# Kernel tuning notes

Hardware: AMD Instinct MI355X
Metric: run time of the kernel (lower is better)

The kernel has to match this reference:

```python
import jax, jax.numpy as jnp
import numpy as np

NUM_HEADS = 16
NEG = -1e9


def setup_inputs() -> dict:
    key = jax.random.key(0)
    k_x, k_w1, k_w2, k_b, k_p = jax.random.split(key, 5)
    B, T, C = 4, 2048, 1024
    x = jax.random.normal(k_x, (B, T, C), dtype=jnp.float32)
    # nn.Linear default init ~ U(-1/sqrt(fan_in), 1/sqrt(fan_in)); stored as (in, out) for x @ W
    s = 1.0 / np.sqrt(C)
    Wqkv = jax.random.uniform(k_w1, (C, 3 * C), minval=-s, maxval=s, dtype=jnp.float32)
    Wout = jax.random.uniform(k_w2, (C, C), minval=-s, maxval=s, dtype=jnp.float32)
    bout = jax.random.uniform(k_b, (C,), minval=-s, maxval=s, dtype=jnp.float32)
    perm = jax.random.permutation(k_p, T).astype(jnp.int32)
    return {"x": x, "Wqkv": Wqkv, "Wout": Wout, "bout": bout, "perm": perm}


def reference(x, Wqkv, Wout, bout, perm):
    B, T, C = x.shape
    H = NUM_HEADS
    D = C // H
    qkv = x @ Wqkv                                   # [B,T,3C]
    q, k, v = jnp.split(qkv, 3, axis=-1)
    q = q.reshape(B, T, H, D)
    k = k.reshape(B, T, H, D)
    v = v.reshape(B, T, H, D)
    scale = 1.0 / jnp.sqrt(jnp.asarray(D, dtype=x.dtype))
    scores = jnp.einsum('bqhd,bkhd->bhqk', q, k) * scale   # [B,H,T,T]
    # permuted causal mask: allowed[i, j] = tril[i, perm[j]] = (perm[j] <= i)
    i = jnp.arange(T)[:, None]
    bias = jnp.where(perm[None, :] <= i, 0.0, NEG).astype(x.dtype)  # [T,T]
    attn = jax.nn.softmax(scores + bias[None, None, :, :], axis=-1)
    out = jnp.einsum('bhqk,bkhd->bqhd', attn, v).reshape(B, T, C)
    return out @ Wout + bout
```

## Files before the change

kernel.cpp:

```cpp
#include <hip/hip_runtime.h>
#include <stdint.h>
#include <stddef.h>

#define BSZ   4
#define TSEQ  2048
#define CDIM  1024
#define HEADS 16
#define DHEAD 64

typedef __attribute__((ext_vector_type(8))) short v8s;
typedef __attribute__((ext_vector_type(4))) float v4f;

__device__ __forceinline__ v4f mfma16(v8s a, v8s b, v4f c) {
  return __builtin_amdgcn_mfma_f32_16x16x32_bf16(a, b, c, 0, 0, 0);
}

__device__ __forceinline__ short f2bf(float f) {
  union { float f; uint32_t u; } v; v.f = f;
  uint32_t r = (v.u + 0x7FFFu + ((v.u >> 16) & 1u)) >> 16;
  return (short)(uint16_t)r;
}

__device__ __forceinline__ uint32_t cvt_pk_bf16(float lo, float hi) {
  uint32_t r;
  asm("v_cvt_pk_bf16_f32 %0, %1, %2" : "=v"(r) : "v"(lo), "v"(hi));
  return r;
}

__device__ __forceinline__ void gl_lds16(const void* g, void* l) {
  __builtin_amdgcn_global_load_lds((const __attribute__((address_space(1))) void*)g,
                                   (__attribute__((address_space(3))) void*)l, 16, 0, 0);
}

#define BARw __builtin_amdgcn_s_barrier()
#define LGKM0 do { asm volatile("s_waitcnt lgkmcnt(0)" ::: "memory"); \
                   __builtin_amdgcn_sched_barrier(0); } while (0)

__global__ __launch_bounds__(256) void k_convert(const float* __restrict__ in,
                                                 short* __restrict__ out, int n) {
  int i = (blockIdx.x * 256 + threadIdx.x) * 4;
  if (i >= n) return;
  float4 v = *(const float4*)(in + i);
  short4 o;
  o.x = f2bf(v.x); o.y = f2bf(v.y); o.z = f2bf(v.z); o.w = f2bf(v.w);
  *(short4*)(out + i) = o;
}

__global__ __launch_bounds__(256) void k_transpose_conv(const float* __restrict__ in,
                                                        short* __restrict__ out,
                                                        int R, int C) {
  __shared__ float tile[32][33];
  int c0 = blockIdx.x * 32, r0 = blockIdx.y * 32;
  int tx = threadIdx.x, ty = threadIdx.y;
  #pragma unroll
  for (int i = ty; i < 32; i += 8)
    tile[i][tx] = in[(size_t)(r0 + i) * C + c0 + tx];
  __syncthreads();
  #pragma unroll
  for (int i = ty; i < 32; i += 8)
    out[(size_t)(c0 + i) * R + r0 + tx] = f2bf(tile[tx][i]);
}

__global__ __launch_bounds__(256) void k_vt(const short* __restrict__ Vs,
                                            short* __restrict__ Vt) {
  __shared__ short tl[64][72];
  const int t0 = blockIdx.x * 64, h = blockIdx.y, b = blockIdx.z;
  const int row = threadIdx.x >> 2, c4 = threadIdx.x & 3;
  const short* src = Vs + (size_t)(b * TSEQ + t0 + row) * CDIM + h * DHEAD;
  #pragma unroll
  for (int it = 0; it < 2; ++it) {
    int ch = c4 + it * 4;
    *(v8s*)&tl[row][ch * 8] = *(const v8s*)(src + ch * 8);
  }
  __syncthreads();
  short* dst = Vt + ((size_t)(b * HEADS + h) * DHEAD + row) * TSEQ + t0;
  #pragma unroll
  for (int it = 0; it < 2; ++it) {
    int ch = c4 + it * 4;
    v8s o;
    #pragma unroll
    for (int j = 0; j < 8; ++j) o[j] = tl[ch * 8 + j][row];
    *(v8s*)(dst + ch * 8) = o;
  }
}

__global__ __launch_bounds__(512, 2) void k_gemm_qkv(const short* __restrict__ A,
                                                     const short* __restrict__ Wt,
                                                     const int* __restrict__ perm,
                                                     short* __restrict__ QK,
                                                     short* __restrict__ Vs) {
  __shared__ __align__(16) short Alds[2][256 * 64];
  __shared__ __align__(16) short Blds[2][256 * 64];
  const int l = threadIdx.x & 63, w = threadIdx.x >> 6;
  const int lr = l & 15, lg = l >> 4;
  const int wm = w >> 2, wn = w & 3;
  const int bid = blockIdx.x;
  const int swz = (bid & 7) * 48 + (bid >> 3);
  const int by = swz / 12, bx = swz - by * 12;
  const int row0 = by * 256, col0 = bx * 256;

  v4f acc[8][4];
  #pragma unroll
  for (int i = 0; i < 8; ++i)
    #pragma unroll
    for (int j = 0; j < 4; ++j) acc[i][j] = (v4f){0.f, 0.f, 0.f, 0.f};

  const int rowoff = w * 8 + (l >> 3);
  const int gch = ((l & 7) ^ (l >> 3)) * 16;
  const char* Asrc = (const char*)A  + (size_t)(row0 + rowoff) * 2048 + gch;
  const char* Bsrc = (const char*)Wt + (size_t)(col0 + rowoff) * 2048 + gch;
  char* AL = (char*)&Alds[0][0];
  char* BL = (char*)&Blds[0][0];
  const int sdst = w * 1024;

  auto SA = [&](int kt, int h, int d) {
    char* dst = AL + d * 32768 + h * 16384 + sdst;
    const char* s = Asrc + (size_t)(h * 128) * 2048 + kt * 128;
    gl_lds16(s, dst);
    gl_lds16(s + (size_t)64 * 2048, dst + 8192);
  };
  auto SB = [&](int kt, int h, int d) {
    char* dst = BL + d * 32768 + h * 16384 + sdst;
    const char* s = Bsrc + (size_t)(h * 128) * 2048 + kt * 128;
    gl_lds16(s, dst);
    gl_lds16(s + (size_t)64 * 2048, dst + 8192);
  };

  const int rsw = (lr & 7) * 16;
  const int koff0 = (lg * 16) ^ rsw;
  const int koff1 = ((4 + lg) * 16) ^ rsw;
  const int abase = (wm * 128 + lr) * 128;
  const int bbase = (wn * 64 + lr) * 128;

  v8s af[4][2], bf[4][2];
  auto RDA = [&](int d, int ih) {
    const char* base = AL + d * 32768 + abase + ih * 8192;
    #pragma unroll
    for (int ii = 0; ii < 4; ++ii) {
      af[ii][0] = *(const v8s*)(base + ii * 2048 + koff0);
      af[ii][1] = *(const v8s*)(base + ii * 2048 + koff1);
    }
  };
  auto RDB = [&](int d) {
    const char* base = BL + d * 32768 + bbase;
    #pragma unroll
    for (int j = 0; j < 4; ++j) {
      bf[j][0] = *(const v8s*)(base + j * 2048 + koff0);
      bf[j][1] = *(const v8s*)(base + j * 2048 + koff1);
    }
  };

#define MMC(IH, JH)                                                            \
  do {                                                                         \
    __builtin_amdgcn_s_setprio(1);                                             \
    _Pragma("unroll")                                                          \
    for (int kk = 0; kk < 2; ++kk)                                             \
      _Pragma("unroll")                                                        \
      for (int ii = 0; ii < 4; ++ii)                                           \
        _Pragma("unroll")                                                      \
        for (int jj = 0; jj < 2; ++jj)                                         \
          acc[(IH) * 4 + ii][(JH) * 2 + jj] =                                  \
              mfma16(af[ii][kk], bf[(JH) * 2 + jj][kk],                        \
                     acc[(IH) * 4 + ii][(JH) * 2 + jj]);                       \
    __builtin_amdgcn_s_setprio(0);                                             \
  } while (0)

  SB(0, 0, 0); SB(0, 1, 0); SA(0, 0, 0); SA(0, 1, 0);
  SB(1, 0, 1); SB(1, 1, 1); SA(1, 0, 1); SA(1, 1, 1);
  asm volatile("s_waitcnt vmcnt(8)" ::: "memory");
  BARw;

  for (int i = 0; i < 8; ++i) {
    const int kt2 = 2 * i + 2, kt3 = 2 * i + 3;
    const bool st = (i < 7);
    RDA(0, 0); RDB(0);
    BARw; LGKM0; MMC(0, 0); BARw;
    if (st) SB(kt2, 0, 0);
    BARw; MMC(0, 1); BARw;
    RDA(0, 1); if (st) SB(kt2, 1, 0);
    BARw; LGKM0; MMC(1, 0); BARw;
    if (st) { SA(kt2, 0, 0); asm volatile("s_waitcnt vmcnt(6)" ::: "memory"); }
    else    { asm volatile("s_waitcnt vmcnt(0)" ::: "memory"); }
    BARw; MMC(1, 1); BARw;
    RDA(1, 0); RDB(1); if (st) SA(kt2, 1, 0);
    BARw; LGKM0; MMC(0, 0); BARw;
    if (st) SB(kt3, 0, 1);
    BARw; MMC(0, 1); BARw;
    RDA(1, 1); if (st) SB(kt3, 1, 1);
    BARw; LGKM0; MMC(1, 0); BARw;
    if (st) {
      SA(kt3, 0, 1); SA(kt3, 1, 1);
      asm volatile("s_waitcnt vmcnt(8)" ::: "memory");
    }
    BARw; MMC(1, 1); BARw;
  }
#undef MMC

  const int region = (col0 + wn * 64) >> 10;
  if (region == 0) {
    #pragma unroll
    for (int i = 0; i < 8; ++i) {
      int rowb = row0 + wm * 128 + i * 16 + lg * 4;
      #pragma unroll
      for (int j = 0; j < 4; ++j) {
        int col = col0 + wn * 64 + j * 16 + lr;
        #pragma unroll
        for (int r = 0; r < 4; ++r)
          QK[(size_t)(rowb + r) * 2048 + col] = f2bf(acc[i][j][r]);
      }
    }
  } else if (region == 1) {
    #pragma unroll
    for (int i = 0; i < 8; ++i) {
      int rowb = row0 + wm * 128 + i * 16 + lg * 4;
      int prow[4];
      #pragma unroll
      for (int r = 0; r < 4; ++r) {
        int t = (rowb + r) & 2047;
        prow[r] = ((rowb + r) - t) + perm[t];
      }
      #pragma unroll
      for (int j = 0; j < 4; ++j) {
        int col = col0 + wn * 64 + j * 16 + lr;
        #pragma unroll
        for (int r = 0; r < 4; ++r)
          QK[(size_t)prow[r] * 2048 + col] = f2bf(acc[i][j][r]);
      }
    }
  } else {
    #pragma unroll
    for (int i = 0; i < 8; ++i) {
      int rowb = row0 + wm * 128 + i * 16 + lg * 4;
      int prow[4];
      #pragma unroll
      for (int r = 0; r < 4; ++r) {
        int t = (rowb + r) & 2047;
        prow[r] = ((rowb + r) - t) + perm[t];
      }
      #pragma unroll
      for (int j = 0; j < 4; ++j) {
        int vc = col0 + wn * 64 + j * 16 + lr - 2048;
        #pragma unroll
        for (int r = 0; r < 4; ++r)
          Vs[(size_t)prow[r] * CDIM + vc] = f2bf(acc[i][j][r]);
      }
    }
  }
}

__global__ __launch_bounds__(256) void k_gemm_out(const short* __restrict__ A,
                                                  const short* __restrict__ Wt,
                                                  const float* __restrict__ bias,
                                                  float* __restrict__ out) {
  __shared__ __align__(16) short As[3][128 * 32];
  __shared__ __align__(16) short Bs[3][128 * 32];
  int l = threadIdx.x & 63, w = threadIdx.x >> 6;
  int lr = l & 15, lg = l >> 4;
  int row0 = blockIdx.y * 128, col0 = blockIdx.x * 128;
  int wr = (w >> 1) * 64, wc = (w & 1) * 64;
  v4f acc[4][4];
  #pragma unroll
  for (int i = 0; i < 4; ++i)
    #pragma unroll
    for (int j = 0; j < 4; ++j) acc[i][j] = (v4f){0.f, 0.f, 0.f, 0.f};

  const short* Ag = A  + (size_t)(row0 + w * 32 + (l >> 2)) * CDIM + (l & 3) * 8;
  const short* Bg = Wt + (size_t)(col0 + w * 32 + (l >> 2)) * CDIM + (l & 3) * 8;
  const int so = (w * 32) * 32;

  auto STAGE = [&](int it, int bf) {
    int k0 = it * 32;
    gl_lds16(Ag + k0, &As[bf][so]);
    gl_lds16(Ag + k0 + 16 * CDIM, &As[bf][so + 16 * 32]);
    gl_lds16(Bg + k0, &Bs[bf][so]);
    gl_lds16(Bg + k0 + 16 * CDIM, &Bs[bf][so + 16 * 32]);
  };

  auto BODY = [&](int it, int cur) {
    if (it < 31) asm volatile("s_waitcnt vmcnt(4)" ::: "memory");
    else         asm volatile("s_waitcnt vmcnt(0)" ::: "memory");
    __builtin_amdgcn_s_barrier();
    if (it < 30) STAGE(it + 2, (cur + 2) % 3);
    v8s af[4], bfr[4];
    #pragma unroll
    for (int i = 0; i < 4; ++i) af[i] = *(const v8s*)&As[cur][(wr + i * 16 + lr) * 32 + lg * 8];
    #pragma unroll
    for (int j = 0; j < 4; ++j) bfr[j] = *(const v8s*)&Bs[cur][(wc + j * 16 + lr) * 32 + lg * 8];
    __builtin_amdgcn_s_setprio(1);
    #pragma unroll
    for (int i = 0; i < 4; ++i)
      #pragma unroll
      for (int j = 0; j < 4; ++j) acc[i][j] = mfma16(af[i], bfr[j], acc[i][j]);
    __builtin_amdgcn_s_setprio(0);
  };

  STAGE(0, 0);
  STAGE(1, 1);
  for (int it = 0; it < 30; it += 3) {
    BODY(it, 0); BODY(it + 1, 1); BODY(it + 2, 2);
  }
  BODY(30, 0);
  BODY(31, 1);

  #pragma unroll
  for (int i = 0; i < 4; ++i) {
    int rowb = row0 + wr + i * 16 + lg * 4;
    #pragma unroll
    for (int j = 0; j < 4; ++j) {
      int col = col0 + wc + j * 16 + lr;
      float bv = bias[col];
      #pragma unroll
      for (int r = 0; r < 4; ++r)
        out[(size_t)(rowb + r) * CDIM + col] = acc[i][j][r] + bv;
    }
  }
}

__global__ __launch_bounds__(512) void k_flash(const short* __restrict__ QK,
                                               const short* __restrict__ Vt,
                                               short* __restrict__ O) {
  __shared__ __align__(16) short Kbuf[3][64 * 64];
  __shared__ __align__(16) short Vbuf[3][64 * 64];
  __shared__ __align__(16) short plds[8][32 * 64];
  const int l = threadIdx.x & 63, w = threadIdx.x >> 6;
  const int lr = l & 15, lg = l >> 4;
  const int n = blockIdx.x;
  const int u = n & 255;
  const int h = u & 15;
  const int b = (u >> 4) & 3;
  const int qi = u >> 6;
  const int qb = (n < 256) ? (7 - qi) : qi;
  const int q0 = qb * 256 + w * 32;
  const int nt = 4 * qb + 4;
  const float C1 = 0.18033688011112042f;

  const short* Qb = QK + (size_t)(b * TSEQ + q0) * 2048 + h * DHEAD;
  v8s aq[2][2];
  #pragma unroll
  for (int hh = 0; hh < 2; ++hh) {
    aq[hh][0] = *(const v8s*)(Qb + (size_t)(hh * 16 + lr) * 2048 + lg * 8);
    aq[hh][1] = *(const v8s*)(Qb + (size_t)(hh * 16 + lr) * 2048 + 32 + lg * 8);
  }

  v8s ones;
  #pragma unroll
  for (int i = 0; i < 8; ++i) ones[i] = (short)0x3F80;

  v4f Oacc[2][4], sacc[2];
  #pragma unroll
  for (int hh = 0; hh < 2; ++hh) {
    sacc[hh] = (v4f){0.f, 0.f, 0.f, 0.f};
    #pragma unroll
    for (int d = 0; d < 4; ++d) Oacc[hh][d] = (v4f){0.f, 0.f, 0.f, 0.f};
  }

  const char* Ksrc = (const char*)QK + (size_t)(b * TSEQ) * 4096 + 2048 + (size_t)h * 128;
  const char* Vsrc = (const char*)Vt + (size_t)((b * HEADS + h) * DHEAD) * 4096;
  const int srow = w * 8 + (l >> 3);
  const int csw  = ((l & 7) ^ (l >> 3)) * 16;

  auto STAGE = [&](int kt, int bf) {
    char* kd = (char*)&Kbuf[bf][0] + w * 1024;
    char* vd = (char*)&Vbuf[bf][0] + w * 1024;
    gl_lds16(Ksrc + ((size_t)kt * 64 + srow) * 4096 + csw, kd);
    gl_lds16(Vsrc + (size_t)srow * 4096 + (size_t)kt * 128 + csw, vd);
  };

  STAGE(0, 0);
  if (nt > 1) STAGE(1, 1);
  const int x16 = (lr & 7) * 16;
  char* pb = (char*)&plds[w][0];
  const int e7 = lr & 7;

  for (int kt = 0; kt < nt; ++kt) {
    const int cur = kt % 3;
    if (kt + 1 < nt) asm volatile("s_waitcnt vmcnt(2)" ::: "memory");
    else             asm volatile("s_waitcnt vmcnt(0)" ::: "memory");
    __builtin_amdgcn_s_barrier();
    if (kt + 2 < nt) STAGE(kt + 2, (kt + 2) % 3);

    if (kt * 64 <= q0 + 31) {
      const char* Kc = (const char*)&Kbuf[cur][0];
      const char* Vc = (const char*)&Vbuf[cur][0];

      v4f S[2][4];
      __builtin_amdgcn_s_setprio(1);
      #pragma unroll
      for (int g = 0; g < 4; ++g) {
        const char* rp = Kc + (g * 16 + lr) * 128;
        v8s k0 = *(const v8s*)(rp + ((lg * 16) ^ x16));
        v8s k1 = *(const v8s*)(rp + ((64 + lg * 16) ^ x16));
        #pragma unroll
        for (int hh = 0; hh < 2; ++hh) {
          v4f z = (v4f){0.f, 0.f, 0.f, 0.f};
          z = mfma16(k0, aq[hh][0], z);
          S[hh][g] = mfma16(k1, aq[hh][1], z);
        }
      }
      __builtin_amdgcn_s_setprio(0);

      if (kt * 64 + 63 <= q0) {
        #pragma unroll
        for (int hh = 0; hh < 2; ++hh) {
          char* rowp = pb + (hh * 16 + lr) * 128 + 8 * (lg & 1);
          #pragma unroll
          for (int g = 0; g < 4; ++g) {
            float p0 = __builtin_exp2f(fmaf(S[hh][g][0], C1, -8.0f));
            float p1 = __builtin_exp2f(fmaf(S[hh][g][1], C1, -8.0f));
            float p2 = __builtin_exp2f(fmaf(S[hh][g][2], C1, -8.0f));
            float p3 = __builtin_exp2f(fmaf(S[hh][g][3], C1, -8.0f));
            uint2 wv;
            wv.x = cvt_pk_bf16(p0, p1);
            wv.y = cvt_pk_bf16(p2, p3);
            *(uint2*)(rowp + (((2 * g + (lg >> 1)) ^ e7) << 4)) = wv;
          }
        }
      } else {
        const int kg0 = kt * 64 + lg * 4;
        #pragma unroll
        for (int hh = 0; hh < 2; ++hh) {
          const int irow = q0 + hh * 16 + lr;
          char* rowp = pb + (hh * 16 + lr) * 128 + 8 * (lg & 1);
          #pragma unroll
          for (int g = 0; g < 4; ++g) {
            float p[4];
            #pragma unroll
            for (int r = 0; r < 4; ++r) {
              float e = __builtin_exp2f(fmaf(S[hh][g][r], C1, -8.0f));
              p[r] = (kg0 + g * 16 + r <= irow) ? e : 0.0f;
            }
            uint2 wv;
            wv.x = cvt_pk_bf16(p[0], p[1]);
            wv.y = cvt_pk_bf16(p[2], p[3]);
            *(uint2*)(rowp + (((2 * g + (lg >> 1)) ^ e7) << 4)) = wv;
          }
        }
      }
      asm volatile("s_waitcnt lgkmcnt(0)" ::: "memory");
      __builtin_amdgcn_sched_barrier(0);

      v8s ap[2][2];
      #pragma unroll
      for (int hh = 0; hh < 2; ++hh) {
        const char* rowp = pb + (hh * 16 + lr) * 128;
        ap[hh][0] = *(const v8s*)(rowp + ((lg ^ e7) << 4));
        ap[hh][1] = *(const v8s*)(rowp + (((4 + lg) ^ e7) << 4));
      }
      __builtin_amdgcn_s_setprio(1);
      #pragma unroll
      for (int hh = 0; hh < 2; ++hh) {
        sacc[hh] = mfma16(ap[hh][0], ones, sacc[hh]);
        sacc[hh] = mfma16(ap[hh][1], ones, sacc[hh]);
      }
      #pragma unroll
      for (int dk = 0; dk < 4; ++dk) {
        const char* vp = Vc + (dk * 16 + lr) * 128;
        v8s bv0 = *(const v8s*)(vp + ((lg * 16) ^ x16));
        v8s bv1 = *(const v8s*)(vp + ((64 + lg * 16) ^ x16));
        #pragma unroll
        for (int hh = 0; hh < 2; ++hh) {
          Oacc[hh][dk] = mfma16(ap[hh][0], bv0, Oacc[hh][dk]);
          Oacc[hh][dk] = mfma16(ap[hh][1], bv1, Oacc[hh][dk]);
        }
      }
      __builtin_amdgcn_s_setprio(0);
    }
  }

  #pragma unroll
  for (int hh = 0; hh < 2; ++hh) {
    float inv[4];
    #pragma unroll
    for (int r = 0; r < 4; ++r) inv[r] = 1.0f / sacc[hh][r];
    #pragma unroll
    for (int dk = 0; dk < 4; ++dk)
      #pragma unroll
      for (int r = 0; r < 4; ++r) {
        int row = q0 + hh * 16 + lg * 4 + r;
        int col = h * DHEAD + dk * 16 + lr;
        O[(size_t)(b * TSEQ + row) * CDIM + col] = f2bf(Oacc[hh][dk][r] * inv[r]);
      }
  }
}

extern "C" void kernel_launch(void* const* d_in, const int* in_sizes, int n_in,
                              void* d_out, int out_size, void* d_ws, size_t ws_size,
                              hipStream_t stream) {
  const float* x    = (const float*)d_in[0];
  const float* Wqkv = (const float*)d_in[1];
  const float* Wout = (const float*)d_in[2];
  const float* bout = (const float*)d_in[3];
  const int*   perm = (const int*)d_in[4];
  float* out = (float*)d_out;

  uint8_t* ws = (uint8_t*)d_ws;
  const size_t NTOK = (size_t)BSZ * TSEQ;
  size_t off = 0;
  short* Xb    = (short*)(ws + off); off += NTOK * CDIM * 2;
  short* Wqkvt = (short*)(ws + off); off += (size_t)3 * CDIM * CDIM * 2;
  short* Woutt = (short*)(ws + off); off += (size_t)CDIM * CDIM * 2;
  short* QKb   = (short*)(ws + off); off += NTOK * 2048 * 2;
  short* Vtb   = (short*)(ws + off); off += NTOK * CDIM * 2;
  short* Obuf  = (short*)(ws + off); off += NTOK * CDIM * 2;
  short* Vsb   = Obuf;

  {
    int n = (int)(NTOK * CDIM);
    k_convert<<<n / (256 * 4), 256, 0, stream>>>(x, Xb, n);
  }
  k_transpose_conv<<<dim3(3 * CDIM / 32, CDIM / 32), dim3(32, 8), 0, stream>>>(Wqkv, Wqkvt, CDIM, 3 * CDIM);
  k_transpose_conv<<<dim3(CDIM / 32, CDIM / 32), dim3(32, 8), 0, stream>>>(Wout, Woutt, CDIM, CDIM);
  k_gemm_qkv<<<dim3((NTOK / 256) * (3 * CDIM / 256)), 512, 0, stream>>>(Xb, Wqkvt, perm, QKb, Vsb);
  k_vt<<<dim3(TSEQ / 64, HEADS, BSZ), 256, 0, stream>>>(Vsb, Vtb);
  k_flash<<<dim3(512), 512, 0, stream>>>(QKb, Vtb, Obuf);
  k_gemm_out<<<dim3(CDIM / 128, NTOK / 128), 256, 0, stream>>>(Obuf, Woutt, bout, out);
}
```

Before: 201.4 us.

## Split long causal query blocks across two KV halves and add combine kernel

The attention kernel splits the key range of the four heaviest query blocks (upper half of the sequence) into two halves, each processed by a separate workgroup. Partial unnormalized outputs and row sums go to scratch buffers, and a new combine kernel adds them and normalizes. The aim is to balance load across a larger grid (768 blocks instead of 512) and shorten the critical path. The cost is an extra launch, the scratch traffic, and rounding the partials to bf16 before they are summed. The scheme relies on fixed softmax without a running max, so partial sums can be added directly.

```diff
diff --git a/kernel.cpp b/kernel.cpp
--- a/kernel.cpp
+++ b/kernel.cpp
@@ -19,6 +19,11 @@
   union { float f; uint32_t u; } v; v.f = f;
   uint32_t r = (v.u + 0x7FFFu + ((v.u >> 16) & 1u)) >> 16;
   return (short)(uint16_t)r;
+}
+
+__device__ __forceinline__ float bf2f(short s) {
+  union { float f; uint32_t u; } v; v.u = ((uint32_t)(uint16_t)s) << 16;
+  return v.f;
 }
 
 __device__ __forceinline__ uint32_t cvt_pk_bf16(float lo, float hi) {
@@ -318,20 +323,27 @@
 
 __global__ __launch_bounds__(512) void k_flash(const short* __restrict__ QK,
                                                const short* __restrict__ Vt,
-                                               short* __restrict__ O) {
+                                               short* __restrict__ O,
+                                               short* __restrict__ Opart,
+                                               float* __restrict__ Spart) {
   __shared__ __align__(16) short Kbuf[3][64 * 64];
   __shared__ __align__(16) short Vbuf[3][64 * 64];
   __shared__ __align__(16) short plds[8][32 * 64];
   const int l = threadIdx.x & 63, w = threadIdx.x >> 6;
   const int lr = l & 15, lg = l >> 4;
   const int n = blockIdx.x;
-  const int u = n & 255;
+  const int grp = n >> 6;
+  const int u = n & 63;
   const int h = u & 15;
-  const int b = (u >> 4) & 3;
-  const int qi = u >> 6;
-  const int qb = (n < 256) ? (7 - qi) : qi;
+  const int b = u >> 4;
+  const bool spl = (grp < 8);
+  const int qb   = spl ? (7 - (grp >> 1)) : (11 - grp);
+  const int half = spl ? (grp & 1) : 0;
+  const int ntf  = 4 * qb + 4;
+  const int kt0  = (spl && half) ? (ntf >> 1) : 0;
+  const int kt1  = (spl && !half) ? (ntf >> 1) : ntf;
+  const int ntl  = kt1 - kt0;
   const int q0 = qb * 256 + w * 32;
-  const int nt = 4 * qb + 4;
   const float C1 = 0.18033688011112042f;
 
   const short* Qb = QK + (size_t)(b * TSEQ + q0) * 2048 + h * DHEAD;
@@ -366,18 +378,19 @@
     gl_lds16(Vsrc + (size_t)srow * 4096 + (size_t)kt * 128 + csw, vd);
   };
 
-  STAGE(0, 0);
-  if (nt > 1) STAGE(1, 1);
+  STAGE(kt0, 0);
+  if (ntl > 1) STAGE(kt0 + 1, 1);
   const int x16 = (lr & 7) * 16;
   char* pb = (char*)&plds[w][0];
   const int e7 = lr & 7;
 
-  for (int kt = 0; kt < nt; ++kt) {
-    const int cur = kt % 3;
-    if (kt + 1 < nt) asm volatile("s_waitcnt vmcnt(2)" ::: "memory");
+  for (int j = 0; j < ntl; ++j) {
+    const int kt = kt0 + j;
+    const int cur = j % 3;
+    if (j + 1 < ntl) asm volatile("s_waitcnt vmcnt(2)" ::: "memory");
     else             asm volatile("s_waitcnt vmcnt(0)" ::: "memory");
     __builtin_amdgcn_s_barrier();
-    if (kt + 2 < nt) STAGE(kt + 2, (kt + 2) % 3);
+    if (j + 2 < ntl) STAGE(kt0 + j + 2, (j + 2) % 3);
 
     if (kt * 64 <= q0 + 31) {
       const char* Kc = (const char*)&Kbuf[cur][0];
@@ -467,20 +480,62 @@
     }
   }
 
-  #pragma unroll
-  for (int hh = 0; hh < 2; ++hh) {
-    float inv[4];
-    #pragma unroll
-    for (int r = 0; r < 4; ++r) inv[r] = 1.0f / sacc[hh][r];
-    #pragma unroll
-    for (int dk = 0; dk < 4; ++dk)
-      #pragma unroll
-      for (int r = 0; r < 4; ++r) {
-        int row = q0 + hh * 16 + lg * 4 + r;
-        int col = h * DHEAD + dk * 16 + lr;
-        O[(size_t)(b * TSEQ + row) * CDIM + col] = f2bf(Oacc[hh][dk][r] * inv[r]);
-      }
-  }
+  if (!spl) {
+    #pragma unroll
+    for (int hh = 0; hh < 2; ++hh) {
+      float inv[4];
+      #pragma unroll
+      for (int r = 0; r < 4; ++r) inv[r] = 1.0f / sacc[hh][r];
+      #pragma unroll
+      for (int dk = 0; dk < 4; ++dk)
+        #pragma unroll
+        for (int r = 0; r < 4; ++r) {
+          int row = q0 + hh * 16 + lg * 4 + r;
+          int col = h * DHEAD + dk * 16 + lr;
+          O[(size_t)(b * TSEQ + row) * CDIM + col] = f2bf(Oacc[hh][dk][r] * inv[r]);
+        }
+    }
+  } else {
+    #pragma unroll
+    for (int hh = 0; hh < 2; ++hh)
+      #pragma unroll
+      for (int dk = 0; dk < 4; ++dk)
+        #pragma unroll
+        for (int r = 0; r < 4; ++r) {
+          int prow = q0 + hh * 16 + lg * 4 + r - 1024;
+          int col = h * DHEAD + dk * 16 + lr;
+          Opart[((size_t)(half * 4 + b) * 1024 + prow) * 1024 + col] = f2bf(Oacc[hh][dk][r]);
+        }
+    if (lr == 0) {
+      #pragma unroll
+      for (int hh = 0; hh < 2; ++hh)
+        #pragma unroll
+        for (int r = 0; r < 4; ++r) {
+          int prow = q0 + hh * 16 + lg * 4 + r - 1024;
+          Spart[((size_t)(half * 4 + b) * 16 + h) * 1024 + prow] = sacc[hh][r];
+        }
+    }
+  }
+}
+
+__global__ __launch_bounds__(256) void k_combine(const short* __restrict__ Opart,
+                                                 const float* __restrict__ Spart,
+                                                 short* __restrict__ O) {
+  int idx = (blockIdx.x * 256 + threadIdx.x) * 8;
+  int row = idx >> 10;
+  int col = idx & 1023;
+  int b = row >> 10, pr = row & 1023;
+  int h = col >> 6;
+  float s = Spart[((size_t)b * 16 + h) * 1024 + pr] +
+            Spart[((size_t)(4 + b) * 16 + h) * 1024 + pr];
+  float inv = 1.0f / s;
+  v8s o0 = *(const v8s*)(Opart + ((size_t)row) * 1024 + col);
+  v8s o1 = *(const v8s*)(Opart + ((size_t)(4096 + row)) * 1024 + col);
+  v8s o;
+  #pragma unroll
+  for (int j = 0; j < 8; ++j)
+    o[j] = f2bf((bf2f(o0[j]) + bf2f(o1[j])) * inv);
+  *(v8s*)(O + ((size_t)(b * TSEQ + 1024 + pr)) * 1024 + col) = o;
 }
 
 extern "C" void kernel_launch(void* const* d_in, const int* in_sizes, int n_in,
@@ -502,7 +557,9 @@
   short* QKb   = (short*)(ws + off); off += NTOK * 2048 * 2;
   short* Vtb   = (short*)(ws + off); off += NTOK * CDIM * 2;
   short* Obuf  = (short*)(ws + off); off += NTOK * CDIM * 2;
+  float* Spart = (float*)(ws + off); off += 2 * 4 * 16 * 1024 * 4;
   short* Vsb   = Obuf;
+  short* Opart = Xb;
 
   {
     int n = (int)(NTOK * CDIM);
@@ -512,6 +569,7 @@
   k_transpose_conv<<<dim3(CDIM / 32, CDIM / 32), dim3(32, 8), 0, stream>>>(Wout, Woutt, CDIM, CDIM);
   k_gemm_qkv<<<dim3((NTOK / 256) * (3 * CDIM / 256)), 512, 0, stream>>>(Xb, Wqkvt, perm, QKb, Vsb);
   k_vt<<<dim3(TSEQ / 64, HEADS, BSZ), 256, 0, stream>>>(Vsb, Vtb);
-  k_flash<<<dim3(512), 512, 0, stream>>>(QKb, Vtb, Obuf);
+  k_flash<<<dim3(768), 512, 0, stream>>>(QKb, Vtb, Obuf, Opart, Spart);
+  k_combine<<<dim3(2048), 256, 0, stream>>>(Opart, Spart, Obuf);
   k_gemm_out<<<dim3(CDIM / 128, NTOK / 128), 256, 0, stream>>>(Obuf, Woutt, bout, out);
 }
```

Result: slower. 206.8 us (+2.6%).
